# Optimization experiments

Hardware: AMD Instinct MI355X
Metric: run time of the kernel (lower is better)

Reference implementation:

```python
import jax, jax.numpy as jnp
import numpy as np

EMBED = 1024
HEADS = 16
HEAD_DIM = EMBED // HEADS
BASE = 10000.0


def _rope_cos_sin(seq_len, dim, dtype):
    inv_freq = 1.0 / (BASE ** (jnp.arange(0, dim, 2, dtype=jnp.float32) / dim))
    t = jnp.arange(seq_len, dtype=jnp.float32)
    freqs = jnp.einsum('i,j->ij', t, inv_freq)           # [S, dim/2]
    emb = jnp.concatenate([freqs, freqs], axis=-1)        # [S, dim]
    return jnp.cos(emb).astype(dtype), jnp.sin(emb).astype(dtype)


def _rotate_half(x):
    d = x.shape[-1] // 2
    return jnp.concatenate([-x[..., d:], x[..., :d]], axis=-1)


def setup_inputs() -> dict:
    key = jax.random.key(0)
    ks = jax.random.split(key, 7)
    B, S = 2, 2048
    scale = 0.02
    return {
        'query': jax.random.normal(ks[0], (B, S, EMBED), jnp.float32),
        'key': jax.random.normal(ks[1], (B, S, EMBED), jnp.float32),
        'value': jax.random.normal(ks[2], (B, S, EMBED), jnp.float32),
        'Wq': jax.random.normal(ks[3], (EMBED, EMBED), jnp.float32) * scale,
        'Wk': jax.random.normal(ks[4], (EMBED, EMBED), jnp.float32) * scale,
        'Wv': jax.random.normal(ks[5], (EMBED, EMBED), jnp.float32) * scale,
        'Wo': jax.random.normal(ks[6], (EMBED, EMBED), jnp.float32) * scale,
    }


def reference(query, key, value, Wq, Wk, Wv, Wo):
    B, Sq, _ = query.shape
    Sk = key.shape[1]
    # projections (bias-free Linear: x @ W^T; W sampled so use x @ W directly)
    q = (query @ Wq).reshape(B, Sq, HEADS, HEAD_DIM).transpose(0, 2, 1, 3)  # [B,H,Sq,Dh]
    k = (key @ Wk).reshape(B, Sk, HEADS, HEAD_DIM).transpose(0, 2, 1, 3)
    v = (value @ Wv).reshape(B, Sk, HEADS, HEAD_DIM).transpose(0, 2, 1, 3)
    # RoPE applied to q and k per-position
    cos_q, sin_q = _rope_cos_sin(Sq, HEAD_DIM, q.dtype)  # [Sq,Dh]
    cos_k, sin_k = _rope_cos_sin(Sk, HEAD_DIM, k.dtype)
    q = q * cos_q[None, None] + _rotate_half(q) * sin_q[None, None]
    k = k * cos_k[None, None] + _rotate_half(k) * sin_k[None, None]
    scores = jnp.einsum('bhqd,bhkd->bhqk', q, k) / jnp.sqrt(jnp.asarray(HEAD_DIM, q.dtype))
    probs = jax.nn.softmax(scores, axis=-1)
    out = jnp.einsum('bhqk,bhkd->bhqd', probs, v)
    out = out.transpose(0, 2, 1, 3).reshape(B, Sq, EMBED)
    return out @ Wo
```

## Files before the change

kernel.cpp:

```cpp
#include <hip/hip_runtime.h>
#include <hip/hip_bf16.h>


typedef unsigned short u16;
typedef unsigned int u32;
typedef __attribute__((ext_vector_type(8))) short short8;
typedef __attribute__((ext_vector_type(4))) float f32x4;

#define MFMA16(a, b, c) __builtin_amdgcn_mfma_f32_16x16x32_bf16((a), (b), (c), 0, 0, 0)

typedef __attribute__((address_space(3))) u16 lds_u16;
typedef __attribute__((address_space(1))) const u16 glb_u16;

__device__ __forceinline__ void gload16(const u16* g, u16* l) {
    __builtin_amdgcn_global_load_lds((glb_u16*)g, (lds_u16*)l, 16, 0, 0);
}

__device__ __forceinline__ u16 f2bf(float f) {
    __hip_bfloat16 h = __float2bfloat16(f);
    return *reinterpret_cast<u16*>(&h);
}

__global__ __launch_bounds__(256) void conv_x(const float* __restrict__ q,
                                              const float* __restrict__ k,
                                              const float* __restrict__ v,
                                              u16* __restrict__ X3) {
    int z = blockIdx.y;
    const float* src = (z == 0) ? q : (z == 1) ? k : v;
    int i = (blockIdx.x * 256 + threadIdx.x) * 4;
    float4 f = *reinterpret_cast<const float4*>(src + i);
    ushort4 o;
    o.x = f2bf(f.x); o.y = f2bf(f.y); o.z = f2bf(f.z); o.w = f2bf(f.w);
    *reinterpret_cast<ushort4*>(X3 + (size_t)z * 4194304 + i) = o;
}

__global__ __launch_bounds__(256) void transpose_w(const float* __restrict__ w0,
                                                   const float* __restrict__ w1,
                                                   const float* __restrict__ w2,
                                                   const float* __restrict__ w3,
                                                   u16* __restrict__ WT) {
    __shared__ float t[32][33];
    const float* Ws[4] = {w0, w1, w2, w3};
    const float* W = Ws[blockIdx.z];
    int n0 = blockIdx.x * 32, k0 = blockIdx.y * 32;
    int tx = threadIdx.x, ty = threadIdx.y;
    for (int r = 0; r < 4; r++) {
        int kk = ty + r * 8;
        t[kk][tx] = W[(k0 + kk) * 1024 + n0 + tx];
    }
    __syncthreads();
    u16* out = WT + (size_t)blockIdx.z * 1048576;
    for (int r = 0; r < 4; r++) {
        int nn = ty + r * 8;
        out[(n0 + nn) * 1024 + k0 + tx] = f2bf(t[tx][nn]);
    }
}

__global__ __launch_bounds__(256) void rope_table(float2* __restrict__ tab) {
    int gid = blockIdx.x * 256 + threadIdx.x;
    int s = gid >> 5, d = gid & 31;
    float inv = powf(10000.f, -(float)d / 32.f);
    float fr = (float)s * inv;
    tab[gid] = make_float2(cosf(fr), sinf(fr));
}

__global__ __launch_bounds__(256) void gemm_qkv(const u16* __restrict__ Aall,
                                                const u16* __restrict__ WT,
                                                u16* __restrict__ Qp,
                                                u16* __restrict__ Kf,
                                                u16* __restrict__ Vf,
                                                const float2* __restrict__ tab) {
    int z = blockIdx.z;
    const u16* A  = Aall + (size_t)z * 4194304;
    const u16* Bt = WT + (size_t)z * 1048576;
    const int K = 1024;
    int m0 = blockIdx.y * 128, n0 = blockIdx.x * 128;
    __shared__ u16 As[128 * 32];
    __shared__ u16 Bs[128 * 32];
    int tid = threadIdx.x;
    int wave = tid >> 6, lane = tid & 63, quad = lane >> 4, l16 = lane & 15;
    int wm = (wave >> 1) * 64, wn = (wave & 1) * 64;
    f32x4 acc[4][4];
    for (int i = 0; i < 4; i++)
        for (int j = 0; j < 4; j++)
            for (int r = 0; r < 4; r++) acc[i][j][r] = 0.f;

    for (int k0 = 0; k0 < K; k0 += 32) {
        __syncthreads();
        for (int c = 0; c < 2; c++) {
            int e = (tid + c * 256) * 8;
            int row = e >> 5, col = e & 31;
            gload16(&A[(size_t)(m0 + row) * K + k0 + col], &As[e]);
            gload16(&Bt[(size_t)(n0 + row) * K + k0 + col], &Bs[e]);
        }
        __syncthreads();
        short8 af[4], bfr[4];
        for (int i = 0; i < 4; i++)
            af[i] = *reinterpret_cast<const short8*>(&As[(wm + i * 16 + l16) * 32 + quad * 8]);
        for (int j = 0; j < 4; j++)
            bfr[j] = *reinterpret_cast<const short8*>(&Bs[(wn + j * 16 + l16) * 32 + quad * 8]);
        for (int i = 0; i < 4; i++)
            for (int j = 0; j < 4; j++)
                acc[i][j] = MFMA16(af[i], bfr[j], acc[i][j]);
    }

    int h = (n0 + wn) >> 6;
    if (z == 2) {
        for (int i = 0; i < 4; i++) {
            int sbase = m0 + wm + i * 16 + quad * 4;
            int b = sbase >> 11, srel = sbase & 2047;
            int u = srel >> 5, qv = (srel >> 3) & 3, j0 = srel & 7;
            u16* Vbh = Vf + ((size_t)(b * 16 + h)) * 131072;
            for (int j = 0; j < 4; j++) {
                ushort4 o;
                o.x = f2bf(acc[i][j][0]);
                o.y = f2bf(acc[i][j][1]);
                o.z = f2bf(acc[i][j][2]);
                o.w = f2bf(acc[i][j][3]);
                *reinterpret_cast<ushort4*>(
                    &Vbh[(size_t)(((u * 4 + j) * 4 + qv) * 128 + l16 * 8 + j0)]) = o;
            }
        }
    } else if (z == 1) {
        for (int i = 0; i < 4; i++)
            for (int r = 0; r < 4; r++) {
                int m = m0 + wm + i * 16 + quad * 4 + r;
                int b = m >> 11, srel = m & 2047;
                int t = srel >> 4, lf = srel & 15;
                u16* Kbh = Kf + ((size_t)(b * 16 + h)) * 131072;
                for (int j2 = 0; j2 < 2; j2++) {
                    int d = j2 * 16 + l16;
                    float2 cs = tab[srel * 32 + d];
                    float x1 = acc[i][j2][r];
                    float x2 = acc[i][j2 + 2][r];
                    int qd = (d >> 3) & 3, j = d & 7;
                    Kbh[(size_t)(((t * 2 + 0) * 4 + qd) * 128 + lf * 8 + j)] =
                        f2bf(x1 * cs.x - x2 * cs.y);
                    Kbh[(size_t)(((t * 2 + 1) * 4 + qd) * 128 + lf * 8 + j)] =
                        f2bf(x2 * cs.x + x1 * cs.y);
                }
            }
    } else {
        for (int i = 0; i < 4; i++)
            for (int r = 0; r < 4; r++) {
                int m = m0 + wm + i * 16 + quad * 4 + r;
                int b = m >> 11, s = m & 2047;
                u16* row = Qp + (((size_t)(b * 16 + h)) * 2048 + s) * 64;
                for (int j2 = 0; j2 < 2; j2++) {
                    int d = j2 * 16 + l16;
                    float2 cs = tab[s * 32 + d];
                    float x1 = acc[i][j2][r] * 0.125f;
                    float x2 = acc[i][j2 + 2][r] * 0.125f;
                    row[d]      = f2bf(x1 * cs.x - x2 * cs.y);
                    row[d + 32] = f2bf(x2 * cs.x + x1 * cs.y);
                }
            }
    }
}

__global__ __launch_bounds__(256) void gemm_bt_f32(const u16* __restrict__ A,
                                                   const u16* __restrict__ Bt,
                                                   float* __restrict__ C,
                                                   int M, int N, int K) {
    int m0 = blockIdx.y * 128, n0 = blockIdx.x * 128;
    __shared__ u16 As[128 * 32];
    __shared__ u16 Bs[128 * 32];
    int tid = threadIdx.x;
    int wave = tid >> 6, lane = tid & 63, quad = lane >> 4, l16 = lane & 15;
    int wm = (wave >> 1) * 64, wn = (wave & 1) * 64;
    f32x4 acc[4][4];
    for (int i = 0; i < 4; i++)
        for (int j = 0; j < 4; j++)
            for (int r = 0; r < 4; r++) acc[i][j][r] = 0.f;

    for (int k0 = 0; k0 < K; k0 += 32) {
        __syncthreads();
        for (int c = 0; c < 2; c++) {
            int e = (tid + c * 256) * 8;
            int row = e >> 5, col = e & 31;
            gload16(&A[(size_t)(m0 + row) * K + k0 + col], &As[e]);
            gload16(&Bt[(size_t)(n0 + row) * K + k0 + col], &Bs[e]);
        }
        __syncthreads();
        short8 af[4], bfr[4];
        for (int i = 0; i < 4; i++)
            af[i] = *reinterpret_cast<const short8*>(&As[(wm + i * 16 + l16) * 32 + quad * 8]);
        for (int j = 0; j < 4; j++)
            bfr[j] = *reinterpret_cast<const short8*>(&Bs[(wn + j * 16 + l16) * 32 + quad * 8]);
        for (int i = 0; i < 4; i++)
            for (int j = 0; j < 4; j++)
                acc[i][j] = MFMA16(af[i], bfr[j], acc[i][j]);
    }

    for (int i = 0; i < 4; i++)
        for (int r = 0; r < 4; r++) {
            int m = m0 + wm + i * 16 + quad * 4 + r;
            for (int j = 0; j < 4; j++)
                C[(size_t)m * N + n0 + wn + j * 16 + l16] = acc[i][j][r];
        }
}

__global__ __launch_bounds__(512, 4) void flash_attn(const u16* __restrict__ Qp,
                                                     const u16* __restrict__ Kf,
                                                     const u16* __restrict__ Vf,
                                                     u16* __restrict__ attn) {
    int bh = blockIdx.x, q0 = blockIdx.y * 128;
    const u16* Q  = Qp + (size_t)bh * 131072;
    const u16* Kb = Kf + (size_t)bh * 131072;
    const u16* Vb = Vf + (size_t)bh * 131072;
    __shared__ u16 smem[8 * 32 * 76];
    int tid = threadIdx.x, wave = tid >> 6, lane = tid & 63;
    int quad = lane >> 4, l16 = lane & 15;
    int qg = wave & 3, kh = wave >> 2;
    u16* Pw = smem + wave * (32 * 76);

    short8 qf[2][2];
    for (int g = 0; g < 2; g++)
        for (int kk = 0; kk < 2; kk++)
            qf[g][kk] = *reinterpret_cast<const short8*>(
                &Q[(size_t)(q0 + qg * 32 + g * 16 + l16) * 64 + kk * 32 + quad * 8]);

    float psum[2] = {0.f, 0.f};
    f32x4 Oacc[2][4];
    for (int g = 0; g < 2; g++)
        for (int dt = 0; dt < 4; dt++)
            for (int r = 0; r < 4; r++) Oacc[g][dt][r] = 0.f;

    for (int kv0 = 0; kv0 < 2048; kv0 += 128) {
        f32x4 st[2][4];
        for (int g = 0; g < 2; g++)
            for (int nt = 0; nt < 4; nt++)
                for (int r = 0; r < 4; r++) st[g][nt][r] = 0.f;
        for (int kk = 0; kk < 2; kk++)
            for (int nt = 0; nt < 4; nt++) {
                int t = (kv0 >> 4) + kh * 4 + nt;
                short8 af = *reinterpret_cast<const short8*>(
                    &Kb[(size_t)((t * 2 + kk) * 4) * 128 + lane * 8]);
                for (int g = 0; g < 2; g++)
                    st[g][nt] = MFMA16(af, qf[g][kk], st[g][nt]);
            }

        for (int g = 0; g < 2; g++)
            for (int nt = 0; nt < 4; nt++) {
                float p0 = __expf(st[g][nt][0]);
                float p1 = __expf(st[g][nt][1]);
                float p2 = __expf(st[g][nt][2]);
                float p3 = __expf(st[g][nt][3]);
                psum[g] += (p0 + p1) + (p2 + p3);
                uint2 w;
                w.x = (u32)f2bf(p0) | ((u32)f2bf(p1) << 16);
                w.y = (u32)f2bf(p2) | ((u32)f2bf(p3) << 16);
                *reinterpret_cast<uint2*>(
                    &Pw[(g * 16 + l16) * 76 + nt * 16 + quad * 4]) = w;
            }

        for (int kk = 0; kk < 2; kk++) {
            short8 pa[2];
            for (int g = 0; g < 2; g++)
                pa[g] = *reinterpret_cast<const short8*>(
                    &Pw[(g * 16 + l16) * 76 + kk * 32 + quad * 8]);
            int u = (kv0 >> 5) + kh * 2 + kk;
            for (int dt = 0; dt < 4; dt++) {
                short8 bv = *reinterpret_cast<const short8*>(
                    &Vb[(size_t)((u * 4 + dt) * 4) * 128 + lane * 8]);
                for (int g = 0; g < 2; g++)
                    Oacc[g][dt] = MFMA16(pa[g], bv, Oacc[g][dt]);
            }
        }
    }

    for (int g = 0; g < 2; g++) {
        psum[g] += __shfl_xor(psum[g], 16);
        psum[g] += __shfl_xor(psum[g], 32);
    }

    float* Of = reinterpret_cast<float*>(smem);
    float* ph = Of + 128 * 65;
    __syncthreads();
    if (kh == 1) {
        for (int g = 0; g < 2; g++) {
            for (int dt = 0; dt < 4; dt++)
                for (int r = 0; r < 4; r++)
                    Of[(qg * 32 + g * 16 + quad * 4 + r) * 65 + dt * 16 + l16] = Oacc[g][dt][r];
            if (quad == 0) ph[qg * 32 + g * 16 + l16] = psum[g];
        }
    }
    __syncthreads();
    if (kh == 0) {
        int b = bh >> 4, h = bh & 15;
        for (int g = 0; g < 2; g++) {
            float ps = psum[g] + ph[qg * 32 + g * 16 + l16];
            float linv[4];
            for (int r = 0; r < 4; r++)
                linv[r] = 1.f / __shfl(ps, quad * 4 + r);
            for (int dt = 0; dt < 4; dt++)
                for (int r = 0; r < 4; r++) {
                    float o = Oacc[g][dt][r] +
                              Of[(qg * 32 + g * 16 + quad * 4 + r) * 65 + dt * 16 + l16];
                    int s = q0 + qg * 32 + g * 16 + quad * 4 + r;
                    attn[((size_t)(b * 2048 + s)) * 1024 + h * 64 + dt * 16 + l16] =
                        f2bf(o * linv[r]);
                }
        }
    }
}

extern "C" void kernel_launch(void* const* d_in, const int* in_sizes, int n_in,
                              void* d_out, int out_size, void* d_ws, size_t ws_size,
                              hipStream_t stream) {
    const float* q  = (const float*)d_in[0];
    const float* k  = (const float*)d_in[1];
    const float* v  = (const float*)d_in[2];
    const float* wq = (const float*)d_in[3];
    const float* wk = (const float*)d_in[4];
    const float* wv = (const float*)d_in[5];
    const float* wo = (const float*)d_in[6];

    u16* ws = (u16*)d_ws;
    u16* WT  = ws;
    u16* X3  = ws + (size_t)4 * 1048576;
    u16* QKV = X3 + (size_t)3 * 4194304;
    u16* Qp  = QKV;
    u16* Kf  = QKV + (size_t)1 * 4194304;
    u16* Vf  = QKV + (size_t)2 * 4194304;
    u16* attn = X3;
    float2* tab = (float2*)d_out;

    conv_x<<<dim3(4096, 3), 256, 0, stream>>>(q, k, v, X3);
    transpose_w<<<dim3(32, 32, 4), dim3(32, 8), 0, stream>>>(wq, wk, wv, wo, WT);
    rope_table<<<256, 256, 0, stream>>>(tab);
    gemm_qkv<<<dim3(8, 32, 3), 256, 0, stream>>>(X3, WT, Qp, Kf, Vf, tab);
    flash_attn<<<dim3(32, 16), 512, 0, stream>>>(Qp, Kf, Vf, attn);
    gemm_bt_f32<<<dim3(8, 32, 1), 256, 0, stream>>>(
        attn, WT + (size_t)3 * 1048576, (float*)d_out, 4096, 1024, 1024);
}
```

Baseline: 245.8 us.

## Merge prep kernels, stage Q/K epilogue via LDS, use exp2 and MFMA row sums

The three preprocessing kernels (input conversion, weight transpose, RoPE table) are merged into one launch. The Q/K epilogues of the projection GEMM now stage rotated values through LDS and write 16-byte vectors, and Q is pre-scaled by log2(e)/sqrt(d) so attention can use exp2f. Attention computes row sums with an extra MFMA against a ones vector instead of scalar adds and shuffles, packs bf16 with a cheap rounding shortcut, and walks K/V with incremented pointers. This trades exactness of the bf16 rounding (no NaN handling) and extra MFMA work for less VALU and fewer launches.

```diff
diff --git a/kernel.cpp b/kernel.cpp
--- a/kernel.cpp
+++ b/kernel.cpp
@@ -12,6 +12,8 @@
 typedef __attribute__((address_space(3))) u16 lds_u16;
 typedef __attribute__((address_space(1))) const u16 glb_u16;
 
+#define QSCALE 0.18033688011f
+
 __device__ __forceinline__ void gload16(const u16* g, u16* l) {
     __builtin_amdgcn_global_load_lds((glb_u16*)g, (lds_u16*)l, 16, 0, 0);
 }
@@ -21,47 +23,52 @@
     return *reinterpret_cast<u16*>(&h);
 }
 
-__global__ __launch_bounds__(256) void conv_x(const float* __restrict__ q,
-                                              const float* __restrict__ k,
-                                              const float* __restrict__ v,
-                                              u16* __restrict__ X3) {
-    int z = blockIdx.y;
-    const float* src = (z == 0) ? q : (z == 1) ? k : v;
-    int i = (blockIdx.x * 256 + threadIdx.x) * 4;
-    float4 f = *reinterpret_cast<const float4*>(src + i);
-    ushort4 o;
-    o.x = f2bf(f.x); o.y = f2bf(f.y); o.z = f2bf(f.z); o.w = f2bf(f.w);
-    *reinterpret_cast<ushort4*>(X3 + (size_t)z * 4194304 + i) = o;
-}
-
-__global__ __launch_bounds__(256) void transpose_w(const float* __restrict__ w0,
-                                                   const float* __restrict__ w1,
-                                                   const float* __restrict__ w2,
-                                                   const float* __restrict__ w3,
-                                                   u16* __restrict__ WT) {
+__device__ __forceinline__ u32 pk2(float a, float b) {
+    u32 ua = __float_as_uint(a) + 0x8000u;
+    u32 ub = __float_as_uint(b) + 0x8000u;
+    return (ua >> 16) | (ub & 0xffff0000u);
+}
+
+__global__ __launch_bounds__(256) void prep(const float* __restrict__ q,
+                                            const float* __restrict__ k,
+                                            const float* __restrict__ v,
+                                            const float* __restrict__ w0,
+                                            const float* __restrict__ w1,
+                                            const float* __restrict__ w2,
+                                            const float* __restrict__ w3,
+                                            u16* __restrict__ X3,
+                                            u16* __restrict__ WT,
+                                            float2* __restrict__ tab) {
     __shared__ float t[32][33];
-    const float* Ws[4] = {w0, w1, w2, w3};
-    const float* W = Ws[blockIdx.z];
-    int n0 = blockIdx.x * 32, k0 = blockIdx.y * 32;
-    int tx = threadIdx.x, ty = threadIdx.y;
-    for (int r = 0; r < 4; r++) {
-        int kk = ty + r * 8;
-        t[kk][tx] = W[(k0 + kk) * 1024 + n0 + tx];
-    }
-    __syncthreads();
-    u16* out = WT + (size_t)blockIdx.z * 1048576;
-    for (int r = 0; r < 4; r++) {
-        int nn = ty + r * 8;
-        out[(n0 + nn) * 1024 + k0 + tx] = f2bf(t[tx][nn]);
-    }
-}
-
-__global__ __launch_bounds__(256) void rope_table(float2* __restrict__ tab) {
-    int gid = blockIdx.x * 256 + threadIdx.x;
-    int s = gid >> 5, d = gid & 31;
-    float inv = powf(10000.f, -(float)d / 32.f);
-    float fr = (float)s * inv;
-    tab[gid] = make_float2(cosf(fr), sinf(fr));
+    int blk = blockIdx.x, tid = threadIdx.x;
+    if (blk < 12288) {
+        int z = blk >> 12, xb = blk & 4095;
+        const float* src = (z == 0) ? q : (z == 1) ? k : v;
+        int i = (xb * 256 + tid) * 4;
+        float4 f = *reinterpret_cast<const float4*>(src + i);
+        ushort4 o;
+        o.x = f2bf(f.x); o.y = f2bf(f.y); o.z = f2bf(f.z); o.w = f2bf(f.w);
+        *reinterpret_cast<ushort4*>(X3 + (size_t)z * 4194304 + i) = o;
+    } else if (blk < 16384) {
+        int idx = blk - 12288;
+        int zc = idx & 3;
+        int n0 = ((idx >> 2) & 31) * 32, k0 = (idx >> 7) * 32;
+        const float* Ws[4] = {w0, w1, w2, w3};
+        const float* W = Ws[zc];
+        int tx = tid & 31, ty = tid >> 5;
+        for (int r = 0; r < 4; r++)
+            t[ty + r * 8][tx] = W[(k0 + ty + r * 8) * 1024 + n0 + tx];
+        __syncthreads();
+        u16* out = WT + (size_t)zc * 1048576;
+        for (int r = 0; r < 4; r++)
+            out[(n0 + ty + r * 8) * 1024 + k0 + tx] = f2bf(t[tx][ty + r * 8]);
+    } else {
+        int gid = (blk - 16384) * 256 + tid;
+        int s = gid >> 5, d = gid & 31;
+        float inv = powf(10000.f, -(float)d / 32.f);
+        float fr = (float)s * inv;
+        tab[gid] = make_float2(cosf(fr), sinf(fr));
+    }
 }
 
 __global__ __launch_bounds__(256) void gemm_qkv(const u16* __restrict__ Aall,
@@ -75,8 +82,9 @@
     const u16* Bt = WT + (size_t)z * 1048576;
     const int K = 1024;
     int m0 = blockIdx.y * 128, n0 = blockIdx.x * 128;
-    __shared__ u16 As[128 * 32];
-    __shared__ u16 Bs[128 * 32];
+    __shared__ u16 smem[9216];
+    u16* As = smem;
+    u16* Bs = smem + 4096;
     int tid = threadIdx.x;
     int wave = tid >> 6, lane = tid & 63, quad = lane >> 4, l16 = lane & 15;
     int wm = (wave >> 1) * 64, wn = (wave & 1) * 64;
@@ -121,40 +129,41 @@
                     &Vbh[(size_t)(((u * 4 + j) * 4 + qv) * 128 + l16 * 8 + j0)]) = o;
             }
         }
-    } else if (z == 1) {
-        for (int i = 0; i < 4; i++)
+    } else {
+        __syncthreads();
+        u16* strip = smem + wave * 2304;
+        const float qs = (z == 0) ? QSCALE : 1.f;
+        for (int i = 0; i < 4; i++) {
+            int mb = m0 + wm + i * 16;
+            int b = mb >> 11, srel0 = mb & 2047;
             for (int r = 0; r < 4; r++) {
-                int m = m0 + wm + i * 16 + quad * 4 + r;
-                int b = m >> 11, srel = m & 2047;
-                int t = srel >> 4, lf = srel & 15;
-                u16* Kbh = Kf + ((size_t)(b * 16 + h)) * 131072;
+                int srel = srel0 + quad * 4 + r;
                 for (int j2 = 0; j2 < 2; j2++) {
                     int d = j2 * 16 + l16;
                     float2 cs = tab[srel * 32 + d];
-                    float x1 = acc[i][j2][r];
-                    float x2 = acc[i][j2 + 2][r];
-                    int qd = (d >> 3) & 3, j = d & 7;
-                    Kbh[(size_t)(((t * 2 + 0) * 4 + qd) * 128 + lf * 8 + j)] =
-                        f2bf(x1 * cs.x - x2 * cs.y);
-                    Kbh[(size_t)(((t * 2 + 1) * 4 + qd) * 128 + lf * 8 + j)] =
-                        f2bf(x2 * cs.x + x1 * cs.y);
+                    float x1 = acc[i][j2][r] * qs;
+                    float x2 = acc[i][j2 + 2][r] * qs;
+                    strip[(quad * 4 + r) * 72 + d]      = f2bf(x1 * cs.x - x2 * cs.y);
+                    strip[(quad * 4 + r) * 72 + d + 32] = f2bf(x2 * cs.x + x1 * cs.y);
                 }
             }
-    } else {
-        for (int i = 0; i < 4; i++)
-            for (int r = 0; r < 4; r++) {
-                int m = m0 + wm + i * 16 + quad * 4 + r;
-                int b = m >> 11, s = m & 2047;
-                u16* row = Qp + (((size_t)(b * 16 + h)) * 2048 + s) * 64;
-                for (int j2 = 0; j2 < 2; j2++) {
-                    int d = j2 * 16 + l16;
-                    float2 cs = tab[s * 32 + d];
-                    float x1 = acc[i][j2][r] * 0.125f;
-                    float x2 = acc[i][j2 + 2][r] * 0.125f;
-                    row[d]      = f2bf(x1 * cs.x - x2 * cs.y);
-                    row[d + 32] = f2bf(x2 * cs.x + x1 * cs.y);
+            if (z == 0) {
+                u16* row = Qp + ((size_t)(b * 16 + h) * 2048 + srel0 + l16) * 64;
+                for (int c = 0; c < 2; c++) {
+                    short8 vv = *reinterpret_cast<const short8*>(
+                        &strip[l16 * 72 + c * 32 + quad * 8]);
+                    *reinterpret_cast<short8*>(&row[c * 32 + quad * 8]) = vv;
                 }
-            }
+            } else {
+                int t = srel0 >> 4;
+                u16* Kbh = Kf + (size_t)(b * 16 + h) * 131072;
+                for (int kk = 0; kk < 2; kk++) {
+                    short8 vv = *reinterpret_cast<const short8*>(
+                        &strip[l16 * 72 + kk * 32 + quad * 8]);
+                    *reinterpret_cast<short8*>(&Kbh[(size_t)(t * 2 + kk) * 512 + lane * 8]) = vv;
+                }
+            }
+        }
     }
 }
 
@@ -205,73 +214,72 @@
                                                      const u16* __restrict__ Vf,
                                                      u16* __restrict__ attn) {
     int bh = blockIdx.x, q0 = blockIdx.y * 128;
-    const u16* Q  = Qp + (size_t)bh * 131072;
-    const u16* Kb = Kf + (size_t)bh * 131072;
-    const u16* Vb = Vf + (size_t)bh * 131072;
+    const u16* Q = Qp + (size_t)bh * 131072;
     __shared__ u16 smem[8 * 32 * 76];
     int tid = threadIdx.x, wave = tid >> 6, lane = tid & 63;
     int quad = lane >> 4, l16 = lane & 15;
     int qg = wave & 3, kh = wave >> 2;
     u16* Pw = smem + wave * (32 * 76);
 
+    const u16* kp  = Kf + (size_t)bh * 131072 + kh * 4096 + lane * 8;
+    const u16* kp2 = kp + 2048;
+    const u16* vp  = Vf + (size_t)bh * 131072 + kh * 4096 + lane * 8;
+    const u16* vp2 = vp + 2048;
+
     short8 qf[2][2];
     for (int g = 0; g < 2; g++)
         for (int kk = 0; kk < 2; kk++)
             qf[g][kk] = *reinterpret_cast<const short8*>(
                 &Q[(size_t)(q0 + qg * 32 + g * 16 + l16) * 64 + kk * 32 + quad * 8]);
 
-    float psum[2] = {0.f, 0.f};
-    f32x4 Oacc[2][4];
-    for (int g = 0; g < 2; g++)
+    const f32x4 z4 = {0.f, 0.f, 0.f, 0.f};
+    short8 ones;
+    for (int j = 0; j < 8; j++) ones[j] = (short)0x3F80;
+
+    f32x4 Oacc[2][4], Osum[2];
+    for (int g = 0; g < 2; g++) {
         for (int dt = 0; dt < 4; dt++)
             for (int r = 0; r < 4; r++) Oacc[g][dt][r] = 0.f;
-
-    for (int kv0 = 0; kv0 < 2048; kv0 += 128) {
+        for (int r = 0; r < 4; r++) Osum[g][r] = 0.f;
+    }
+
+    for (int it = 0; it < 16; it++) {
         f32x4 st[2][4];
-        for (int g = 0; g < 2; g++)
-            for (int nt = 0; nt < 4; nt++)
-                for (int r = 0; r < 4; r++) st[g][nt][r] = 0.f;
-        for (int kk = 0; kk < 2; kk++)
-            for (int nt = 0; nt < 4; nt++) {
-                int t = (kv0 >> 4) + kh * 4 + nt;
-                short8 af = *reinterpret_cast<const short8*>(
-                    &Kb[(size_t)((t * 2 + kk) * 4) * 128 + lane * 8]);
-                for (int g = 0; g < 2; g++)
-                    st[g][nt] = MFMA16(af, qf[g][kk], st[g][nt]);
-            }
+        for (int nt = 0; nt < 4; nt++) {
+            const u16* kb = (nt < 2) ? kp : kp2;
+            int off = (nt & 1) * 1024;
+            short8 af0 = *reinterpret_cast<const short8*>(kb + off);
+            short8 af1 = *reinterpret_cast<const short8*>(kb + off + 512);
+            st[0][nt] = MFMA16(af0, qf[0][0], z4);
+            st[0][nt] = MFMA16(af1, qf[0][1], st[0][nt]);
+            st[1][nt] = MFMA16(af0, qf[1][0], z4);
+            st[1][nt] = MFMA16(af1, qf[1][1], st[1][nt]);
+        }
 
         for (int g = 0; g < 2; g++)
             for (int nt = 0; nt < 4; nt++) {
-                float p0 = __expf(st[g][nt][0]);
-                float p1 = __expf(st[g][nt][1]);
-                float p2 = __expf(st[g][nt][2]);
-                float p3 = __expf(st[g][nt][3]);
-                psum[g] += (p0 + p1) + (p2 + p3);
                 uint2 w;
-                w.x = (u32)f2bf(p0) | ((u32)f2bf(p1) << 16);
-                w.y = (u32)f2bf(p2) | ((u32)f2bf(p3) << 16);
+                w.x = pk2(exp2f(st[g][nt][0]), exp2f(st[g][nt][1]));
+                w.y = pk2(exp2f(st[g][nt][2]), exp2f(st[g][nt][3]));
                 *reinterpret_cast<uint2*>(
                     &Pw[(g * 16 + l16) * 76 + nt * 16 + quad * 4]) = w;
             }
 
         for (int kk = 0; kk < 2; kk++) {
-            short8 pa[2];
-            for (int g = 0; g < 2; g++)
-                pa[g] = *reinterpret_cast<const short8*>(
-                    &Pw[(g * 16 + l16) * 76 + kk * 32 + quad * 8]);
-            int u = (kv0 >> 5) + kh * 2 + kk;
+            const u16* vb = kk ? vp2 : vp;
+            short8 pa0 = *reinterpret_cast<const short8*>(
+                &Pw[l16 * 76 + kk * 32 + quad * 8]);
+            short8 pa1 = *reinterpret_cast<const short8*>(
+                &Pw[(16 + l16) * 76 + kk * 32 + quad * 8]);
             for (int dt = 0; dt < 4; dt++) {
-                short8 bv = *reinterpret_cast<const short8*>(
-                    &Vb[(size_t)((u * 4 + dt) * 4) * 128 + lane * 8]);
-                for (int g = 0; g < 2; g++)
-                    Oacc[g][dt] = MFMA16(pa[g], bv, Oacc[g][dt]);
-            }
-        }
-    }
-
-    for (int g = 0; g < 2; g++) {
-        psum[g] += __shfl_xor(psum[g], 16);
-        psum[g] += __shfl_xor(psum[g], 32);
+                short8 bv = *reinterpret_cast<const short8*>(vb + dt * 512);
+                Oacc[0][dt] = MFMA16(pa0, bv, Oacc[0][dt]);
+                Oacc[1][dt] = MFMA16(pa1, bv, Oacc[1][dt]);
+            }
+            Osum[0] = MFMA16(pa0, ones, Osum[0]);
+            Osum[1] = MFMA16(pa1, ones, Osum[1]);
+        }
+        kp += 8192; kp2 += 8192; vp += 8192; vp2 += 8192;
     }
 
     float* Of = reinterpret_cast<float*>(smem);
@@ -282,17 +290,18 @@
             for (int dt = 0; dt < 4; dt++)
                 for (int r = 0; r < 4; r++)
                     Of[(qg * 32 + g * 16 + quad * 4 + r) * 65 + dt * 16 + l16] = Oacc[g][dt][r];
-            if (quad == 0) ph[qg * 32 + g * 16 + l16] = psum[g];
+            if (l16 == 0)
+                for (int r = 0; r < 4; r++)
+                    ph[qg * 32 + g * 16 + quad * 4 + r] = Osum[g][r];
         }
     }
     __syncthreads();
     if (kh == 0) {
         int b = bh >> 4, h = bh & 15;
         for (int g = 0; g < 2; g++) {
-            float ps = psum[g] + ph[qg * 32 + g * 16 + l16];
             float linv[4];
             for (int r = 0; r < 4; r++)
-                linv[r] = 1.f / __shfl(ps, quad * 4 + r);
+                linv[r] = 1.f / (Osum[g][r] + ph[qg * 32 + g * 16 + quad * 4 + r]);
             for (int dt = 0; dt < 4; dt++)
                 for (int r = 0; r < 4; r++) {
                     float o = Oacc[g][dt][r] +
@@ -326,9 +335,7 @@
     u16* attn = X3;
     float2* tab = (float2*)d_out;
 
-    conv_x<<<dim3(4096, 3), 256, 0, stream>>>(q, k, v, X3);
-    transpose_w<<<dim3(32, 32, 4), dim3(32, 8), 0, stream>>>(wq, wk, wv, wo, WT);
-    rope_table<<<256, 256, 0, stream>>>(tab);
+    prep<<<16640, 256, 0, stream>>>(q, k, v, wq, wk, wv, wo, X3, WT, tab);
     gemm_qkv<<<dim3(8, 32, 3), 256, 0, stream>>>(X3, WT, Qp, Kf, Vf, tab);
     flash_attn<<<dim3(32, 16), 512, 0, stream>>>(Qp, Kf, Vf, attn);
     gemm_bt_f32<<<dim3(8, 32, 1), 256, 0, stream>>>(
```

Result: no change. 247.5 us (+0.7%).
